# Kernel tuning notes

Hardware: AMD Instinct MI355X
Metric: run time of the kernel (lower is better)

## Reference

```python
import jax, jax.numpy as jnp
import numpy as np

BN_EPS = 1e-5


def setup_inputs() -> dict:
    key = jax.random.key(0)
    ks = jax.random.split(key, 6)
    B, C, H, W = 4, 256, 64, 64
    Ci = 128
    s_in = 0.02  # small init scale for conv weights
    x = jax.random.normal(ks[0], (B, C, H, W), dtype=jnp.float32)
    g_w = jax.random.normal(ks[1], (Ci, C), dtype=jnp.float32) * s_in
    theta_w = jax.random.normal(ks[2], (Ci, C), dtype=jnp.float32) * s_in
    phi_w = jax.random.normal(ks[3], (Ci, C), dtype=jnp.float32) * s_in
    W_w = jax.random.normal(ks[4], (C, Ci), dtype=jnp.float32) * s_in
    return {
        "x": x,
        "g_w": g_w, "g_b": jnp.zeros((Ci,), jnp.float32),
        "theta_w": theta_w, "theta_b": jnp.zeros((Ci,), jnp.float32),
        "phi_w": phi_w, "phi_b": jnp.zeros((Ci,), jnp.float32),
        "W_w": W_w, "W_b": jnp.zeros((C,), jnp.float32),
        "bn_gamma": jnp.ones((C,), jnp.float32),
        "bn_beta": jnp.zeros((C,), jnp.float32),
    }


def reference(x, g_w, g_b, theta_w, theta_b, phi_w, phi_b, W_w, W_b, bn_gamma, bn_beta):
    B, C, H, W = x.shape
    N = H * W
    xf = x.reshape(B, C, N)  # flatten spatial -> [B, C, N]

    def conv1x1(w, b):  # 1x1 conv == per-position linear over channels
        return jnp.einsum('oc,bcn->bon', w, xf) + b[None, :, None]

    g_x = conv1x1(g_w, g_b)          # [B, Ci, N]
    theta_x = conv1x1(theta_w, theta_b)
    phi_x = conv1x1(phi_w, phi_b)

    f = jnp.einsum('bcn,bcm->bnm', theta_x, phi_x)   # [B, N, N] attention logits
    attn = jax.nn.softmax(f, axis=-1)
    y = jnp.einsum('bnm,bcm->bcn', attn, g_x)        # [B, Ci, N]

    Wy = jnp.einsum('oc,bcn->bon', W_w, y) + W_b[None, :, None]  # [B, C, N]
    Wy = Wy.reshape(B, C, H, W)

    # BatchNorm2d in training mode (default): batch statistics over (B, H, W)
    mean = Wy.mean(axis=(0, 2, 3))
    var = Wy.var(axis=(0, 2, 3))
    Wy_bn = (bn_gamma[None, :, None, None] * (Wy - mean[None, :, None, None])
             * jax.lax.rsqrt(var[None, :, None, None] + BN_EPS)
             + bn_beta[None, :, None, None])
    return Wy_bn + x
```

## Files before the change

kernel.cpp:

```cpp
#include <hip/hip_runtime.h>
#include <hip/hip_bf16.h>

typedef __attribute__((ext_vector_type(8))) __bf16 bf16x8;
typedef __attribute__((ext_vector_type(4))) __bf16 bf16x4;
typedef __attribute__((ext_vector_type(4))) float  f32x4;
typedef __attribute__((ext_vector_type(16))) float f32x16;

#define L2E 1.44269504088896340736f

static __device__ __forceinline__ f32x4 mfma16(bf16x8 a, bf16x8 b, f32x4 c) {
    return __builtin_amdgcn_mfma_f32_16x16x32_bf16(a, b, c, 0, 0, 0);
}
static __device__ __forceinline__ f32x16 mfma32(bf16x8 a, bf16x8 b, f32x16 c) {
    return __builtin_amdgcn_mfma_f32_32x32x16_bf16(a, b, c, 0, 0, 0);
}

#define GLOAD_LDS16(gsrc, ldst)                                                \
    __builtin_amdgcn_global_load_lds(                                          \
        (const __attribute__((address_space(1))) unsigned int*)(gsrc),         \
        (__attribute__((address_space(3))) unsigned int*)(ldst), 16, 0, 0)

__global__ __launch_bounds__(256) void prep_w(
    const float* __restrict__ thw, const float* __restrict__ phw,
    const float* __restrict__ gw,  const float* __restrict__ Ww,
    __bf16* __restrict__ wbf)
{
    const int idx  = blockIdx.x * 256 + threadIdx.x;
    const int base = idx * 4;
    const float* src = (base < 32768) ? thw : (base < 65536) ? phw
                     : (base < 98304) ? gw  : Ww;
    const int off = base & 32767;
    f32x4 v = *reinterpret_cast<const f32x4*>(src + off);
    bf16x4 o;
    #pragma unroll
    for (int i = 0; i < 4; ++i) o[i] = (__bf16)v[i];
    *reinterpret_cast<bf16x4*>(wbf + base) = o;
}

__global__ __launch_bounds__(256, 1) void proj_fused(
    const float* __restrict__ x, const __bf16* __restrict__ wbf,
    const float* __restrict__ bth, const float* __restrict__ bph,
    const float* __restrict__ bg,
    __bf16* __restrict__ thetaT, __bf16* __restrict__ phiT, __bf16* __restrict__ gBlk)
{
    const int b    = blockIdx.y;
    const int n0   = blockIdx.x * 64;
    const int w    = threadIdx.x >> 6;
    const int lane = threadIdx.x & 63;
    const int lo   = lane & 15;
    const int hi   = lane >> 4;
    const int tr   = threadIdx.x >> 4;
    const int tc   = threadIdx.x & 15;

    __shared__ alignas(16) __bf16 XA[64 * 256];
    __shared__ alignas(16) __bf16 WL[128 * 256];
    __shared__ float TF[64][65];

    #pragma unroll 1
    for (int cb = 0; cb < 4; ++cb) {
        if (cb) __syncthreads();
        #pragma unroll
        for (int k = 0; k < 4; ++k) {
            const int cl = k * 16 + tr;
            f32x4 v = *reinterpret_cast<const f32x4*>(
                x + ((size_t)b * 256 + cb * 64 + cl) * 4096 + n0 + tc * 4);
            #pragma unroll
            for (int i = 0; i < 4; ++i) TF[cl][tc * 4 + i] = v[i];
        }
        __syncthreads();
        #pragma unroll
        for (int k = 0; k < 4; ++k) {
            const int nl = k * 16 + tr;
            bf16x4 v;
            #pragma unroll
            for (int i = 0; i < 4; ++i) v[i] = (__bf16)TF[tc * 4 + i][nl];
            const int dst = nl * 512 + ((cb * 128 + tc * 8) ^ ((nl & 7) << 4));
            *reinterpret_cast<bf16x4*>((char*)XA + dst) = v;
        }
    }
    __syncthreads();

    #pragma unroll 1
    for (int p = 0; p < 3; ++p) {
        if (p) __syncthreads();
        #pragma unroll
        for (int u = 0; u < 16; ++u) {
            const int chunk = (w * 16 + u) * 64 + lane;
            const int row   = chunk >> 5;
            const int jb    = (chunk & 31) * 16;
            const int sb    = row * 512 + (jb ^ ((row & 7) << 4));
            GLOAD_LDS16(wbf + p * 32768 + (sb >> 1), &WL[(w * 16 + u) * 512]);
        }
        __syncthreads();

        f32x4 C[8];
        #pragma unroll
        for (int cc = 0; cc < 8; ++cc) C[cc] = f32x4{0.f, 0.f, 0.f, 0.f};

        const int arow = w * 16 + lo;
        #pragma unroll
        for (int kb = 0; kb < 8; ++kb) {
            const int koff = kb * 64 + hi * 16;
            bf16x8 a = *reinterpret_cast<const bf16x8*>(
                (const char*)XA + arow * 512 + (koff ^ ((arow & 7) << 4)));
            bf16x8 bb[8];
            #pragma unroll
            for (int cc = 0; cc < 8; ++cc) {
                const int o = cc * 16 + lo;
                bb[cc] = *reinterpret_cast<const bf16x8*>(
                    (const char*)WL + o * 512 + (koff ^ ((o & 7) << 4)));
            }
            #pragma unroll
            for (int cc = 0; cc < 8; ++cc) C[cc] = mfma16(a, bb[cc], C[cc]);
        }

        const float* bias = (p == 0) ? bth : (p == 1) ? bph : bg;
        if (p < 2) {
            __bf16* out = (p == 0) ? thetaT : phiT;
            const int nbase = n0 + w * 16;
            #pragma unroll
            for (int cc = 0; cc < 8; ++cc) {
                const float bv = bias[cc * 16 + lo];
                #pragma unroll
                for (int r = 0; r < 4; ++r)
                    out[((size_t)b * 4096 + nbase + 4 * hi + r) * 128 + cc * 16 + lo] =
                        (__bf16)(C[cc][r] + bv);
            }
        } else {
            __syncthreads();
            __bf16* T = &XA[0];
            const int nl0 = w * 16 + 4 * hi;
            #pragma unroll
            for (int cc = 0; cc < 8; ++cc) {
                const float bv = bias[cc * 16 + lo];
                #pragma unroll
                for (int r = 0; r < 4; ++r)
                    T[(cc * 16 + lo) * 66 + nl0 + r] = (__bf16)(C[cc][r] + bv);
            }
            __syncthreads();
            #pragma unroll
            for (int q8 = 0; q8 < 8; ++q8) {
                const int qid = q8 * 256 + threadIdx.x;
                const int c   = qid >> 4;
                const int nl  = (qid & 15) * 4;
                const int n   = n0 + nl;
                const int mt  = n >> 5;
                const int mm  = n & 31;
                const int g   = mm >> 2;
                const int gp  = (g & 4) | ((g & 1) << 1) | ((g >> 1) & 1);
                bf16x4 v;
                #pragma unroll
                for (int i = 0; i < 4; ++i) v[i] = T[c * 66 + nl + i];
                *reinterpret_cast<bf16x4*>(
                    gBlk + (((size_t)(b * 128 + mt)) * 128 + c) * 32 + (gp << 2)) = v;
            }
        }
    }
}

template<int NCH>
__global__ __launch_bounds__(256, 3) void attn_kernel(
    const __bf16* __restrict__ thetaT, const __bf16* __restrict__ phiT,
    const __bf16* __restrict__ gBlk, __bf16* __restrict__ yPart,
    float* __restrict__ lPart)
{
    constexpr int SH = (NCH == 8) ? 3 : 2;
    constexpr int NT = (4096 / NCH) / 32;
    const int bid   = blockIdx.x;
    const int chunk = bid & (NCH - 1);
    const int qb    = (bid >> SH) & 31;
    const int b     = bid >> (SH + 5);
    const int w     = threadIdx.x >> 6;
    const int lane  = threadIdx.x & 63;
    const int l31   = lane & 31;
    const int h2    = lane >> 5;
    const int Q0    = qb * 128 + w * 32;
    const int kvbase = chunk * (4096 / NCH);

    __shared__ alignas(16) __bf16 Kt[3][32 * 128];
    __shared__ alignas(16) __bf16 Vt[3][128 * 32];

    bf16x8 qf[8];
    {
        const __bf16* qrow = thetaT + ((size_t)b * 4096 + Q0 + l31) * 128 + h2 * 8;
        #pragma unroll
        for (int ks = 0; ks < 8; ++ks)
            qf[ks] = *reinterpret_cast<const bf16x8*>(qrow + ks * 16);
    }

    f32x16 yacc[4];
    #pragma unroll
    for (int ct = 0; ct < 4; ++ct)
        #pragma unroll
        for (int r = 0; r < 16; ++r) yacc[ct][r] = 0.f;
    float ylrun = 0.f;

    const __bf16* phiB   = phiT + (size_t)b * 4096 * 128;
    const __bf16* gBlk_b = gBlk + (size_t)b * 128 * 4096;

    auto stage = [&](int buf, int t) {
        const int kv = kvbase + t * 32;
        #pragma unroll
        for (int u = 0; u < 2; ++u) {
            const int ii   = w + u * 4;
            const int mrow = ii * 4 + (lane >> 4);
            const int cbl  = ((lane & 15) * 16) ^ ((mrow & 7) << 4);
            const __bf16* src = phiB + ((size_t)(kv + mrow) << 7) + (cbl >> 1);
            GLOAD_LDS16(src, &Kt[buf][ii * 512]);
        }
        const __bf16* vtile = gBlk_b + ((size_t)(kv >> 5) << 12);
        #pragma unroll
        for (int u = 0; u < 2; ++u) {
            const int jj = w + u * 4;
            const int ch = jj * 64 + lane;
            const int c  = ch >> 2;
            const int h  = (ch & 3) ^ ((c >> 1) & 3);
            const __bf16* src = vtile + c * 32 + h * 8;
            GLOAD_LDS16(src, &Vt[buf][jj * 512]);
        }
    };

    stage(0, 0);
    stage(1, 1);

    int ia = 0, ib = 1, ic = 2;
    const int sw = (l31 >> 1) & 3;

    #pragma unroll 1
    for (int t = 0; t < NT; ++t) {
        if (t < NT - 2) {
            stage(ic, t + 2);
            asm volatile("s_waitcnt vmcnt(8)" ::: "memory");
        } else if (t == NT - 2) {
            asm volatile("s_waitcnt vmcnt(4)" ::: "memory");
        } else {
            asm volatile("s_waitcnt vmcnt(0)" ::: "memory");
        }
        __builtin_amdgcn_s_barrier();
        __builtin_amdgcn_sched_barrier(0);

        const char* Kb = (const char*)&Kt[ia][0];
        const char* Vb = (const char*)&Vt[ia][0];

        f32x16 S;
        #pragma unroll
        for (int r = 0; r < 16; ++r) S[r] = 0.f;
        #pragma unroll
        for (int ks = 0; ks < 8; ++ks) {
            bf16x8 ka = *reinterpret_cast<const bf16x8*>(
                Kb + l31 * 256 + ((ks * 32 + h2 * 16) ^ ((l31 & 7) << 4)));
            S = mfma32(ka, qf[ks], S);
        }

        float p[16];
        #pragma unroll
        for (int r = 0; r < 16; ++r) p[r] = __builtin_amdgcn_exp2f(S[r] * L2E);
        float ls = 0.f;
        #pragma unroll
        for (int r = 0; r < 16; ++r) ls += p[r];
        ylrun += ls;
        bf16x8 pa0, pa1;
        #pragma unroll
        for (int e = 0; e < 8; ++e) { pa0[e] = (__bf16)p[e]; pa1[e] = (__bf16)p[8 + e]; }

        #pragma unroll
        for (int ct = 0; ct < 4; ++ct) {
            const int vrow = (ct * 32 + l31) * 64;
            bf16x8 v0 = *reinterpret_cast<const bf16x8*>(Vb + vrow + ((h2 ^ sw) << 4));
            bf16x8 v1 = *reinterpret_cast<const bf16x8*>(Vb + vrow + (((2 + h2) ^ sw) << 4));
            yacc[ct] = mfma32(pa0, v0, yacc[ct]);
            yacc[ct] = mfma32(pa1, v1, yacc[ct]);
        }

        asm volatile("" ::: "memory");
        __builtin_amdgcn_s_barrier();
        __builtin_amdgcn_sched_barrier(0);
        const int tmp = ia; ia = ib; ib = ic; ic = tmp;
    }

    const float ylt = ylrun + __shfl_xor(ylrun, 32);
    const int bc = chunk * 4 + b;
    #pragma unroll
    for (int ct = 0; ct < 4; ++ct)
        #pragma unroll
        for (int r = 0; r < 16; ++r) {
            const int q = Q0 + (r & 3) + 8 * (r >> 2) + 4 * h2;
            yPart[((size_t)bc * 4096 + q) * 128 + ct * 32 + l31] = (__bf16)yacc[ct][r];
        }
    if (h2 == 0)
        lPart[(size_t)bc * 4096 + Q0 + l31] = ylt;
}

template<int NC>
__global__ __launch_bounds__(256) void linv_kernel(
    const float* __restrict__ lPart, float* __restrict__ linv)
{
    const int i = blockIdx.x * 256 + threadIdx.x;
    float s = 0.f;
    #pragma unroll
    for (int c = 0; c < NC; ++c) s += lPart[(size_t)c * 16384 + i];
    linv[i] = 1.0f / s;
}

template<int NC>
__global__ __launch_bounds__(256, 1) void wy_mfma(
    const __bf16* __restrict__ yPart, const float* __restrict__ linv,
    const __bf16* __restrict__ wW, const float* __restrict__ Wb,
    __bf16* __restrict__ Wy, float* __restrict__ pSQ)
{
    const int b    = blockIdx.y;
    const int n0   = blockIdx.x * 64;
    const int w    = threadIdx.x >> 6;
    const int lane = threadIdx.x & 63;
    const int lo   = lane & 15;
    const int hi   = lane >> 4;

    __shared__ alignas(16) __bf16 YL[64 * 128];
    __shared__ alignas(16) __bf16 WL[256 * 128];

    #pragma unroll
    for (int u = 0; u < 16; ++u) {
        const int chunk = (w * 16 + u) * 64 + lane;
        const int row   = chunk >> 4;
        const int jb    = (chunk & 15) * 16;
        const int sb    = row * 256 + (jb ^ ((row & 7) << 4));
        GLOAD_LDS16(wW + (sb >> 1), &WL[(w * 16 + u) * 512]);
    }
    #pragma unroll
    for (int u = 0; u < 4; ++u) {
        const int ch   = u * 256 + threadIdx.x;
        const int row  = ch >> 4;
        const int col8 = ch & 15;
        float acc8[8];
        #pragma unroll
        for (int e = 0; e < 8; ++e) acc8[e] = 0.f;
        #pragma unroll
        for (int c = 0; c < NC; ++c) {
            bf16x8 v = *reinterpret_cast<const bf16x8*>(
                yPart + ((size_t)(c * 4 + b) * 4096 + n0 + row) * 128 + col8 * 8);
            #pragma unroll
            for (int e = 0; e < 8; ++e) acc8[e] += (float)v[e];
        }
        bf16x8 o8;
        #pragma unroll
        for (int e = 0; e < 8; ++e) o8[e] = (__bf16)acc8[e];
        *reinterpret_cast<bf16x8*>(
            (char*)YL + row * 256 + ((col8 * 16) ^ ((row & 7) << 4))) = o8;
    }
    __syncthreads();

    f32x4 C[4][4];
    #pragma unroll
    for (int og = 0; og < 4; ++og)
        #pragma unroll
        for (int ct = 0; ct < 4; ++ct) C[og][ct] = f32x4{0.f, 0.f, 0.f, 0.f};

    #pragma unroll
    for (int kb = 0; kb < 4; ++kb) {
        const int koff = kb * 64 + hi * 16;
        bf16x8 a[4], bb[4];
        #pragma unroll
        for (int og = 0; og < 4; ++og) {
            const int o = w * 64 + og * 16 + lo;
            a[og] = *reinterpret_cast<const bf16x8*>(
                (const char*)WL + o * 256 + (koff ^ ((o & 7) << 4)));
        }
        #pragma unroll
        for (int ct = 0; ct < 4; ++ct) {
            const int nl = ct * 16 + lo;
            bb[ct] = *reinterpret_cast<const bf16x8*>(
                (const char*)YL + nl * 256 + (koff ^ ((nl & 7) << 4)));
        }
        #pragma unroll
        for (int og = 0; og < 4; ++og)
            #pragma unroll
            for (int ct = 0; ct < 4; ++ct)
                C[og][ct] = mfma16(a[og], bb[ct], C[og][ct]);
    }

    float linvv[4];
    #pragma unroll
    for (int ct = 0; ct < 4; ++ct)
        linvv[ct] = linv[b * 4096 + n0 + ct * 16 + lo];

    const int blk = blockIdx.y * 64 + blockIdx.x;
    #pragma unroll
    for (int og = 0; og < 4; ++og)
        #pragma unroll
        for (int r = 0; r < 4; ++r) {
            const int o  = w * 64 + og * 16 + 4 * hi + r;
            const float bv = Wb[o];
            float s = 0.f, q = 0.f;
            #pragma unroll
            for (int ct = 0; ct < 4; ++ct) {
                const float v = C[og][ct][r] * linvv[ct] + bv;
                Wy[((size_t)b * 256 + o) * 4096 + n0 + ct * 16 + lo] = (__bf16)v;
                s += v; q += v * v;
            }
            #pragma unroll
            for (int off = 1; off <= 8; off <<= 1) {
                s += __shfl_xor(s, off);
                q += __shfl_xor(q, off);
            }
            if (lo == 0) {
                pSQ[blk * 256 + o]         = s;
                pSQ[65536 + blk * 256 + o] = q;
            }
        }
}

__global__ __launch_bounds__(256) void stats_finalize(
    const float* __restrict__ pSQ, const float* __restrict__ gamma,
    const float* __restrict__ beta, float* __restrict__ stats)
{
    const int o = blockIdx.x;
    const int t = threadIdx.x;
    float s = pSQ[t * 256 + o];
    float q = pSQ[65536 + t * 256 + o];
    #pragma unroll
    for (int off = 32; off >= 1; off >>= 1) {
        s += __shfl_down(s, off);
        q += __shfl_down(q, off);
    }
    __shared__ float red[8];
    const int wid = t >> 6;
    if ((t & 63) == 0) { red[wid] = s; red[4 + wid] = q; }
    __syncthreads();
    if (t == 0) {
        const float S = red[0] + red[1] + red[2] + red[3];
        const float Q = red[4] + red[5] + red[6] + red[7];
        const float mean = S * (1.f / 16384.f);
        const float var  = Q * (1.f / 16384.f) - mean * mean;
        const float scl  = gamma[o] * rsqrtf(var + 1e-5f);
        stats[o]       = scl;
        stats[256 + o] = beta[o] - mean * scl;
    }
}

__global__ __launch_bounds__(256) void final_kernel(
    const __bf16* __restrict__ Wy, const float* __restrict__ x,
    const float* __restrict__ stats, float* __restrict__ out)
{
    const int idx = blockIdx.x * 256 + threadIdx.x;
    const int o   = (idx >> 10) & 255;
    bf16x4 wyb = *reinterpret_cast<const bf16x4*>(Wy + (size_t)idx * 4);
    f32x4 xv = *reinterpret_cast<const f32x4*>(x + (size_t)idx * 4);
    const float scl = stats[o], sh = stats[256 + o];
    f32x4 res;
    #pragma unroll
    for (int i = 0; i < 4; ++i) res[i] = (float)wyb[i] * scl + sh + xv[i];
    *reinterpret_cast<f32x4*>(out + (size_t)idx * 4) = res;
}

extern "C" void kernel_launch(void* const* d_in, const int* in_sizes, int n_in,
                              void* d_out, int out_size, void* d_ws, size_t ws_size,
                              hipStream_t stream)
{
    const float* x    = (const float*)d_in[0];
    const float* g_w  = (const float*)d_in[1];
    const float* g_b  = (const float*)d_in[2];
    const float* th_w = (const float*)d_in[3];
    const float* th_b = (const float*)d_in[4];
    const float* ph_w = (const float*)d_in[5];
    const float* ph_b = (const float*)d_in[6];
    const float* W_w  = (const float*)d_in[7];
    const float* W_b  = (const float*)d_in[8];
    const float* bn_g = (const float*)d_in[9];
    const float* bn_b = (const float*)d_in[10];
    float* out = (float*)d_out;

    char* ws = (char*)d_ws;
    const size_t MB = 1u << 20;
    __bf16* thetaT = (__bf16*)(ws);
    __bf16* phiT   = (__bf16*)(ws + 4 * MB);
    __bf16* gBlk   = (__bf16*)(ws + 8 * MB);
    __bf16* yPart  = (__bf16*)(ws + 12 * MB);
    __bf16* Wy     = (__bf16*)(ws);
    float*  pSQ    = (float*) (ws + 8 * MB);
    float*  linv   = (float*) (ws + 8 * MB + 524288);

    const bool big = ws_size >= 46926848ull;
    const size_t tail = big ? 44 * MB : 28 * MB;
    float*  lPart = (float*) (ws + tail);
    __bf16* wbf   = (__bf16*)(ws + tail + (big ? 524288 : 262144));
    float*  stats = (float*) (ws + tail + (big ? 786432 : 524288));

    prep_w<<<dim3(128), 256, 0, stream>>>(th_w, ph_w, g_w, W_w, wbf);
    proj_fused<<<dim3(64, 4), 256, 0, stream>>>(
        x, wbf, th_b, ph_b, g_b, thetaT, phiT, gBlk);
    if (big) {
        attn_kernel<8><<<dim3(1024), 256, 0, stream>>>(thetaT, phiT, gBlk, yPart, lPart);
        linv_kernel<8><<<dim3(64), 256, 0, stream>>>(lPart, linv);
        wy_mfma<8><<<dim3(64, 4), 256, 0, stream>>>(yPart, linv, wbf + 98304, W_b, Wy, pSQ);
    } else {
        attn_kernel<4><<<dim3(512), 256, 0, stream>>>(thetaT, phiT, gBlk, yPart, lPart);
        linv_kernel<4><<<dim3(64), 256, 0, stream>>>(lPart, linv);
        wy_mfma<4><<<dim3(64, 4), 256, 0, stream>>>(yPart, linv, wbf + 98304, W_b, Wy, pSQ);
    }
    stats_finalize<<<dim3(256), 256, 0, stream>>>(pSQ, bn_g, bn_b, stats);
    final_kernel<<<dim3(4096), 256, 0, stream>>>(Wy, x, stats, out);
}
```

Measured before the change: 91.03 us.

## Split projection kernel across projections and fold linv into wy_mfma

The projection kernel now launches one block per (spatial tile, projection, batch) instead of looping over the three projections, tripling the grid from 256 to 768 blocks. It halves the weight LDS tile by loading the weights in two halves and aliases the transpose buffer onto it, which allows two blocks per CU. Each block now re-reads and re-transposes its x tile, tripling that traffic. Separately, the small linv_kernel launch is removed and the partial-sum reciprocal is computed inline in wy_mfma, saving one kernel launch at the cost of a few redundant loads.

```diff
diff --git a/kernel.cpp b/kernel.cpp
--- a/kernel.cpp
+++ b/kernel.cpp
@@ -37,13 +37,14 @@
     *reinterpret_cast<bf16x4*>(wbf + base) = o;
 }
 
-__global__ __launch_bounds__(256, 1) void proj_fused(
+__global__ __launch_bounds__(256, 2) void proj_fused(
     const float* __restrict__ x, const __bf16* __restrict__ wbf,
     const float* __restrict__ bth, const float* __restrict__ bph,
     const float* __restrict__ bg,
     __bf16* __restrict__ thetaT, __bf16* __restrict__ phiT, __bf16* __restrict__ gBlk)
 {
-    const int b    = blockIdx.y;
+    const int p    = blockIdx.y;
+    const int b    = blockIdx.z;
     const int n0   = blockIdx.x * 64;
     const int w    = threadIdx.x >> 6;
     const int lane = threadIdx.x & 63;
@@ -53,8 +54,8 @@
     const int tc   = threadIdx.x & 15;
 
     __shared__ alignas(16) __bf16 XA[64 * 256];
-    __shared__ alignas(16) __bf16 WL[128 * 256];
-    __shared__ float TF[64][65];
+    __shared__ alignas(16) __bf16 WL[64 * 256];
+    float* TF = (float*)&WL[0];
 
     #pragma unroll 1
     for (int cb = 0; cb < 4; ++cb) {
@@ -65,7 +66,7 @@
             f32x4 v = *reinterpret_cast<const f32x4*>(
                 x + ((size_t)b * 256 + cb * 64 + cl) * 4096 + n0 + tc * 4);
             #pragma unroll
-            for (int i = 0; i < 4; ++i) TF[cl][tc * 4 + i] = v[i];
+            for (int i = 0; i < 4; ++i) TF[cl * 65 + tc * 4 + i] = v[i];
         }
         __syncthreads();
         #pragma unroll
@@ -73,29 +74,32 @@
             const int nl = k * 16 + tr;
             bf16x4 v;
             #pragma unroll
-            for (int i = 0; i < 4; ++i) v[i] = (__bf16)TF[tc * 4 + i][nl];
+            for (int i = 0; i < 4; ++i) v[i] = (__bf16)TF[(tc * 4 + i) * 65 + nl];
             const int dst = nl * 512 + ((cb * 128 + tc * 8) ^ ((nl & 7) << 4));
             *reinterpret_cast<bf16x4*>((char*)XA + dst) = v;
         }
     }
     __syncthreads();
 
+    const __bf16* wsrc = wbf + p * 32768;
+    f32x4 C[2][4];
+    #pragma unroll
+    for (int hh = 0; hh < 2; ++hh)
+        #pragma unroll
+        for (int cc = 0; cc < 4; ++cc) C[hh][cc] = f32x4{0.f, 0.f, 0.f, 0.f};
+
     #pragma unroll 1
-    for (int p = 0; p < 3; ++p) {
-        if (p) __syncthreads();
-        #pragma unroll
-        for (int u = 0; u < 16; ++u) {
-            const int chunk = (w * 16 + u) * 64 + lane;
+    for (int hh = 0; hh < 2; ++hh) {
+        if (hh) __syncthreads();
+        #pragma unroll
+        for (int u = 0; u < 8; ++u) {
+            const int chunk = (w * 8 + u) * 64 + lane;
             const int row   = chunk >> 5;
             const int jb    = (chunk & 31) * 16;
             const int sb    = row * 512 + (jb ^ ((row & 7) << 4));
-            GLOAD_LDS16(wbf + p * 32768 + (sb >> 1), &WL[(w * 16 + u) * 512]);
+            GLOAD_LDS16(wsrc + hh * 16384 + (sb >> 1), &WL[(w * 8 + u) * 512]);
         }
         __syncthreads();
-
-        f32x4 C[8];
-        #pragma unroll
-        for (int cc = 0; cc < 8; ++cc) C[cc] = f32x4{0.f, 0.f, 0.f, 0.f};
 
         const int arow = w * 16 + lo;
         #pragma unroll
@@ -103,57 +107,62 @@
             const int koff = kb * 64 + hi * 16;
             bf16x8 a = *reinterpret_cast<const bf16x8*>(
                 (const char*)XA + arow * 512 + (koff ^ ((arow & 7) << 4)));
-            bf16x8 bb[8];
-            #pragma unroll
-            for (int cc = 0; cc < 8; ++cc) {
+            bf16x8 bb[4];
+            #pragma unroll
+            for (int cc = 0; cc < 4; ++cc) {
                 const int o = cc * 16 + lo;
                 bb[cc] = *reinterpret_cast<const bf16x8*>(
                     (const char*)WL + o * 512 + (koff ^ ((o & 7) << 4)));
             }
             #pragma unroll
-            for (int cc = 0; cc < 8; ++cc) C[cc] = mfma16(a, bb[cc], C[cc]);
-        }
-
-        const float* bias = (p == 0) ? bth : (p == 1) ? bph : bg;
-        if (p < 2) {
-            __bf16* out = (p == 0) ? thetaT : phiT;
-            const int nbase = n0 + w * 16;
-            #pragma unroll
-            for (int cc = 0; cc < 8; ++cc) {
-                const float bv = bias[cc * 16 + lo];
+            for (int cc = 0; cc < 4; ++cc) C[hh][cc] = mfma16(a, bb[cc], C[hh][cc]);
+        }
+    }
+
+    const float* bias = (p == 0) ? bth : (p == 1) ? bph : bg;
+    if (p < 2) {
+        __bf16* out = (p == 0) ? thetaT : phiT;
+        const int nbase = n0 + w * 16;
+        #pragma unroll
+        for (int hh = 0; hh < 2; ++hh)
+            #pragma unroll
+            for (int cc = 0; cc < 4; ++cc) {
+                const int o  = hh * 64 + cc * 16 + lo;
+                const float bv = bias[o];
                 #pragma unroll
                 for (int r = 0; r < 4; ++r)
-                    out[((size_t)b * 4096 + nbase + 4 * hi + r) * 128 + cc * 16 + lo] =
-                        (__bf16)(C[cc][r] + bv);
+                    out[((size_t)b * 4096 + nbase + 4 * hi + r) * 128 + o] =
+                        (__bf16)(C[hh][cc][r] + bv);
             }
-        } else {
-            __syncthreads();
-            __bf16* T = &XA[0];
-            const int nl0 = w * 16 + 4 * hi;
-            #pragma unroll
-            for (int cc = 0; cc < 8; ++cc) {
-                const float bv = bias[cc * 16 + lo];
+    } else {
+        __syncthreads();
+        __bf16* T = &XA[0];
+        #pragma unroll
+        for (int hh = 0; hh < 2; ++hh)
+            #pragma unroll
+            for (int cc = 0; cc < 4; ++cc) {
+                const int o  = hh * 64 + cc * 16 + lo;
+                const float bv = bias[o];
                 #pragma unroll
                 for (int r = 0; r < 4; ++r)
-                    T[(cc * 16 + lo) * 66 + nl0 + r] = (__bf16)(C[cc][r] + bv);
+                    T[o * 66 + w * 16 + 4 * hi + r] = (__bf16)(C[hh][cc][r] + bv);
             }
-            __syncthreads();
-            #pragma unroll
-            for (int q8 = 0; q8 < 8; ++q8) {
-                const int qid = q8 * 256 + threadIdx.x;
-                const int c   = qid >> 4;
-                const int nl  = (qid & 15) * 4;
-                const int n   = n0 + nl;
-                const int mt  = n >> 5;
-                const int mm  = n & 31;
-                const int g   = mm >> 2;
-                const int gp  = (g & 4) | ((g & 1) << 1) | ((g >> 1) & 1);
-                bf16x4 v;
-                #pragma unroll
-                for (int i = 0; i < 4; ++i) v[i] = T[c * 66 + nl + i];
-                *reinterpret_cast<bf16x4*>(
-                    gBlk + (((size_t)(b * 128 + mt)) * 128 + c) * 32 + (gp << 2)) = v;
-            }
+        __syncthreads();
+        #pragma unroll
+        for (int q8 = 0; q8 < 8; ++q8) {
+            const int qid = q8 * 256 + threadIdx.x;
+            const int c   = qid >> 4;
+            const int nl  = (qid & 15) * 4;
+            const int n   = n0 + nl;
+            const int mt  = n >> 5;
+            const int mm  = n & 31;
+            const int g   = mm >> 2;
+            const int gp  = (g & 4) | ((g & 1) << 1) | ((g >> 1) & 1);
+            bf16x4 v;
+            #pragma unroll
+            for (int i = 0; i < 4; ++i) v[i] = T[c * 66 + nl + i];
+            *reinterpret_cast<bf16x4*>(
+                gBlk + (((size_t)(b * 128 + mt)) * 128 + c) * 32 + (gp << 2)) = v;
         }
     }
 }
@@ -292,19 +301,8 @@
 }
 
 template<int NC>
-__global__ __launch_bounds__(256) void linv_kernel(
-    const float* __restrict__ lPart, float* __restrict__ linv)
-{
-    const int i = blockIdx.x * 256 + threadIdx.x;
-    float s = 0.f;
-    #pragma unroll
-    for (int c = 0; c < NC; ++c) s += lPart[(size_t)c * 16384 + i];
-    linv[i] = 1.0f / s;
-}
-
-template<int NC>
 __global__ __launch_bounds__(256, 1) void wy_mfma(
-    const __bf16* __restrict__ yPart, const float* __restrict__ linv,
+    const __bf16* __restrict__ yPart, const float* __restrict__ lPart,
     const __bf16* __restrict__ wW, const float* __restrict__ Wb,
     __bf16* __restrict__ Wy, float* __restrict__ pSQ)
 {
@@ -380,8 +378,13 @@
 
     float linvv[4];
     #pragma unroll
-    for (int ct = 0; ct < 4; ++ct)
-        linvv[ct] = linv[b * 4096 + n0 + ct * 16 + lo];
+    for (int ct = 0; ct < 4; ++ct) {
+        const int n = b * 4096 + n0 + ct * 16 + lo;
+        float s = 0.f;
+        #pragma unroll
+        for (int c = 0; c < NC; ++c) s += lPart[(size_t)c * 16384 + n];
+        linvv[ct] = 1.0f / s;
+    }
 
     const int blk = blockIdx.y * 64 + blockIdx.x;
     #pragma unroll
@@ -477,7 +480,6 @@
     __bf16* yPart  = (__bf16*)(ws + 12 * MB);
     __bf16* Wy     = (__bf16*)(ws);
     float*  pSQ    = (float*) (ws + 8 * MB);
-    float*  linv   = (float*) (ws + 8 * MB + 524288);
 
     const bool big = ws_size >= 46926848ull;
     const size_t tail = big ? 44 * MB : 28 * MB;
@@ -486,16 +488,14 @@
     float*  stats = (float*) (ws + tail + (big ? 786432 : 524288));
 
     prep_w<<<dim3(128), 256, 0, stream>>>(th_w, ph_w, g_w, W_w, wbf);
-    proj_fused<<<dim3(64, 4), 256, 0, stream>>>(
+    proj_fused<<<dim3(64, 3, 4), 256, 0, stream>>>(
         x, wbf, th_b, ph_b, g_b, thetaT, phiT, gBlk);
     if (big) {
         attn_kernel<8><<<dim3(1024), 256, 0, stream>>>(thetaT, phiT, gBlk, yPart, lPart);
-        linv_kernel<8><<<dim3(64), 256, 0, stream>>>(lPart, linv);
-        wy_mfma<8><<<dim3(64, 4), 256, 0, stream>>>(yPart, linv, wbf + 98304, W_b, Wy, pSQ);
+        wy_mfma<8><<<dim3(64, 4), 256, 0, stream>>>(yPart, lPart, wbf + 98304, W_b, Wy, pSQ);
     } else {
         attn_kernel<4><<<dim3(512), 256, 0, stream>>>(thetaT, phiT, gBlk, yPart, lPart);
-        linv_kernel<4><<<dim3(64), 256, 0, stream>>>(lPart, linv);
-        wy_mfma<4><<<dim3(64, 4), 256, 0, stream>>>(yPart, linv, wbf + 98304, W_b, Wy, pSQ);
+        wy_mfma<4><<<dim3(64, 4), 256, 0, stream>>>(yPart, lPart, wbf + 98304, W_b, Wy, pSQ);
     }
     stats_finalize<<<dim3(256), 256, 0, stream>>>(pSQ, bn_g, bn_b, stats);
     final_kernel<<<dim3(4096), 256, 0, stream>>>(Wy, x, stats, out);
```

Result: slower. 103.1 us (+13.3%).
